# Kernel optimization log

Hardware: AMD Instinct MI355X
Metric: run time of the kernel (lower is better)

The kernel has to match this reference:

```python
import jax, jax.numpy as jnp
import numpy as np

BETA = 0.9      # membrane decay
THRESH = 1.0    # firing threshold


def _lif(x):
    """Leaky integrate-and-fire over leading time axis. x: (T, ..., C) -> spikes (T, ..., C)."""
    def step(mem, xt):
        mem = BETA * mem + xt
        s = (mem > THRESH).astype(xt.dtype)
        mem = mem - s * THRESH  # soft reset
        return mem, s
    _, spikes = jax.lax.scan(step, jnp.zeros_like(x[0]), x)
    return spikes


def setup_inputs() -> dict:
    key = jax.random.key(0)
    k1, k2, k3, k4, k5 = jax.random.split(key, 5)
    T, N, D = 4, 8192, 1024
    E, EF, TOPK = 8, 512, 2  # expert_ff = d_ff // n_experts = 4096 // 8
    x = jax.random.normal(k1, (T, N, D), dtype=jnp.float32)
    expert_indices = jax.random.randint(k2, (N, TOPK), 0, E)
    expert_weights = jax.random.uniform(k3, (N, TOPK), dtype=jnp.float32)
    up_w = jax.random.normal(k4, (E, EF, D), dtype=jnp.float32) * 0.02   # Linear(d_model, ef).weight
    down_w = jax.random.normal(k5, (E, D, EF), dtype=jnp.float32) * 0.02  # Linear(ef, d_model).weight
    return {"x": x, "expert_indices": expert_indices, "expert_weights": expert_weights,
            "up_w": up_w, "down_w": down_w}


def reference(x, expert_indices, expert_weights, up_w, down_w):
    T, N, D = x.shape
    E = up_w.shape[0]
    # Dense combine weights W[n, e] = sum_k weights[n, k] * (indices[n, k] == e)
    W = jnp.zeros((N, E), dtype=x.dtype).at[
        jnp.arange(N)[:, None], expert_indices].add(expert_weights)
    out = jnp.zeros_like(x)
    for e in range(E):  # fixed small loop over experts
        h = _lif(jnp.einsum('tnd,fd->tnf', x, up_w[e]))   # up-proj + LIF hidden
        o = _lif(jnp.einsum('tnf,df->tnd', h, down_w[e]))  # down-proj + LIF output
        out = out + o * W[:, e][None, :, None]             # weighted combine (0 for inactive)
    return out
```

## Files before the change

kernel.cpp:

```cpp
#include <hip/hip_runtime.h>
#include <stdint.h>

#define T_STEPS 4
#define NTOK    8192
#define DMODEL  1024
#define NEXP    8
#define EFF     512
#define BMT     128
#define CAPTOT  (2*NTOK + NEXP*BMT)

typedef __attribute__((ext_vector_type(8))) short bf8_t;
typedef __attribute__((ext_vector_type(4))) float f32x4;

#define MFMA(a,b,c) __builtin_amdgcn_mfma_f32_16x16x32_bf16((a),(b),(c),0,0,0)


__device__ __forceinline__ unsigned short bf16rn(float f) {
    unsigned u = __float_as_uint(f);
    unsigned r = u + 0x7fffu + ((u >> 16) & 1u);
    return (unsigned short)(r >> 16);
}
__device__ __forceinline__ float bf2f(unsigned short h) {
    return __uint_as_float(((unsigned)h) << 16);
}
__device__ __forceinline__ unsigned pk(unsigned short a, unsigned short b) {
    return (unsigned)a | ((unsigned)b << 16);
}

__device__ __forceinline__ void stage8_3limb(const float* __restrict__ src,
                                             unsigned short* d0, unsigned short* d1,
                                             unsigned short* d2) {
    float v[8];
    *(float4*)&v[0] = *(const float4*)(src + 0);
    *(float4*)&v[4] = *(const float4*)(src + 4);
    unsigned short h[8], m[8], l[8];
#pragma unroll
    for (int i = 0; i < 8; ++i) {
        unsigned short a = bf16rn(v[i]);
        float r1 = v[i] - bf2f(a);
        unsigned short b = bf16rn(r1);
        float r2 = r1 - bf2f(b);
        h[i] = a; m[i] = b; l[i] = bf16rn(r2);
    }
    *(uint4*)d0 = make_uint4(pk(h[0],h[1]), pk(h[2],h[3]), pk(h[4],h[5]), pk(h[6],h[7]));
    *(uint4*)d1 = make_uint4(pk(m[0],m[1]), pk(m[2],m[3]), pk(m[4],m[5]), pk(m[6],m[7]));
    *(uint4*)d2 = make_uint4(pk(l[0],l[1]), pk(l[2],l[3]), pk(l[4],l[5]), pk(l[6],l[7]));
}


__global__ void k_count(const int* __restrict__ idx, int* __restrict__ counts) {
    int n = blockIdx.x * blockDim.x + threadIdx.x;
    if (n >= NTOK) return;
    int e0 = idx[2*n], e1 = idx[2*n+1];
    atomicAdd(&counts[e0], 1);
    if (e1 != e0) atomicAdd(&counts[e1], 1);
}

__global__ void k_prefix(const int* __restrict__ counts, int* __restrict__ offsets) {
    if (threadIdx.x == 0) {
        int o = 0;
        for (int e = 0; e < NEXP; ++e) {
            offsets[e] = o;
            o += (counts[e] + BMT - 1) / BMT * BMT;
        }
        offsets[NEXP] = o;
    }
}

__global__ void k_fill(const int* __restrict__ idx, const float* __restrict__ wts,
                       const int* __restrict__ offsets, int* __restrict__ cursors,
                       int* __restrict__ tok, float* __restrict__ wgt) {
    int n = blockIdx.x * blockDim.x + threadIdx.x;
    if (n >= NTOK) return;
    int e0 = idx[2*n], e1 = idx[2*n+1];
    float w0 = wts[2*n], w1 = wts[2*n+1];
    if (e0 == e1) w0 = __fadd_rn(w0, w1);
    int p0 = offsets[e0] + atomicAdd(&cursors[e0], 1);
    tok[p0] = n; wgt[p0] = w0;
    if (e1 != e0) {
        int p1 = offsets[e1] + atomicAdd(&cursors[e1], 1);
        tok[p1] = n; wgt[p1] = w1;
    }
}


__global__ __launch_bounds__(256, 2)
void k_up(const float* __restrict__ x, const float* __restrict__ up_w,
          const int* __restrict__ offsets, const int* __restrict__ tok,
          unsigned short* __restrict__ spk) {
    const int m0 = blockIdx.x * BMT;
    const int ft = blockIdx.y;
    if (m0 >= offsets[NEXP]) return;
    int e = 0;
    for (int i = 1; i < NEXP; ++i) if (m0 >= offsets[i]) e = i;

    __shared__ unsigned short As[3][128][40];
    __shared__ unsigned short Bs[3][128][40];

    const int tid  = threadIdx.x;
    const int lane = tid & 63, wid = tid >> 6;
    const int quad = lane >> 4, l16 = lane & 15;
    const int mw = (wid & 1) * 64, nw = (wid >> 1) * 64;

    const int r = tid >> 1, half = tid & 1;
    const int tokA = tok[m0 + r];
    const float* xbase = x + (size_t)tokA * DMODEL + half * 16;
    const float* wrow  = up_w + ((size_t)e * EFF + ft * 128 + r) * DMODEL + half * 16;

    f32x4 mem[4][4];
#pragma unroll
    for (int i = 0; i < 4; ++i)
#pragma unroll
        for (int j = 0; j < 4; ++j) mem[i][j] = (f32x4){0.f,0.f,0.f,0.f};

    for (int t = 0; t < T_STEPS; ++t) {
        f32x4 acc[4][4];
#pragma unroll
        for (int i = 0; i < 4; ++i)
#pragma unroll
            for (int j = 0; j < 4; ++j) acc[i][j] = (f32x4){0.f,0.f,0.f,0.f};

        const float* xrow = xbase + (size_t)t * NTOK * DMODEL;

        for (int kc = 0; kc < DMODEL; kc += 32) {
            __syncthreads();
            stage8_3limb(xrow + kc,     &As[0][r][half*16],   &As[1][r][half*16],   &As[2][r][half*16]);
            stage8_3limb(xrow + kc + 8, &As[0][r][half*16+8], &As[1][r][half*16+8], &As[2][r][half*16+8]);
            stage8_3limb(wrow + kc,     &Bs[0][r][half*16],   &Bs[1][r][half*16],   &Bs[2][r][half*16]);
            stage8_3limb(wrow + kc + 8, &Bs[0][r][half*16+8], &Bs[1][r][half*16+8], &Bs[2][r][half*16+8]);
            __syncthreads();

            bf8_t bh[4], bm[4], bl[4];
#pragma unroll
            for (int nt = 0; nt < 4; ++nt) {
                const int nr = nw + nt*16 + l16;
                bh[nt] = *(const bf8_t*)&Bs[0][nr][quad*8];
                bm[nt] = *(const bf8_t*)&Bs[1][nr][quad*8];
                bl[nt] = *(const bf8_t*)&Bs[2][nr][quad*8];
            }
#pragma unroll
            for (int mt = 0; mt < 4; ++mt) {
                const int mr = mw + mt*16 + l16;
                bf8_t ah = *(const bf8_t*)&As[0][mr][quad*8];
                bf8_t am = *(const bf8_t*)&As[1][mr][quad*8];
                bf8_t al = *(const bf8_t*)&As[2][mr][quad*8];
#pragma unroll
                for (int nt = 0; nt < 4; ++nt) {
                    f32x4 c = acc[mt][nt];
                    c = MFMA(ah, bh[nt], c);
                    c = MFMA(am, bh[nt], c);
                    c = MFMA(ah, bm[nt], c);
                    c = MFMA(am, bm[nt], c);
                    c = MFMA(al, bh[nt], c);
                    c = MFMA(ah, bl[nt], c);
                    acc[mt][nt] = c;
                }
            }
        }

#pragma unroll
        for (int mt = 0; mt < 4; ++mt)
#pragma unroll
            for (int nt = 0; nt < 4; ++nt)
#pragma unroll
                for (int reg = 0; reg < 4; ++reg) {
                    float mv = __fadd_rn(__fmul_rn(0.9f, mem[mt][nt][reg]), acc[mt][nt][reg]);
                    bool s = mv > 1.0f;
                    mem[mt][nt][reg] = __fsub_rn(mv, s ? 1.0f : 0.0f);
                    int row = m0 + mw + mt*16 + quad*4 + reg;
                    int col = ft*128 + nw + nt*16 + l16;
                    spk[((size_t)t * CAPTOT + row) * EFF + col] = s ? 0x3F80u : 0u;
                }
    }
}


__global__ __launch_bounds__(256, 3)
void k_dn(const unsigned short* __restrict__ spk, const float* __restrict__ down_w,
          const int* __restrict__ offsets, const int* __restrict__ tok,
          const float* __restrict__ wgt, float* __restrict__ out) {
    const int m0 = blockIdx.x * BMT;
    const int dt = blockIdx.y;
    if (m0 >= offsets[NEXP]) return;
    int e = 0;
    for (int i = 1; i < NEXP; ++i) if (m0 >= offsets[i]) e = i;

    __shared__ unsigned short As[128][40];
    __shared__ unsigned short Bs[3][64][40];

    const int tid  = threadIdx.x;
    const int lane = tid & 63, wid = tid >> 6;
    const int quad = lane >> 4, l16 = lane & 15;
    const int mw = (wid & 1) * 64, nw = (wid >> 1) * 32;

    const int r = tid >> 1, half = tid & 1;
    const int dr = tid >> 2, q = tid & 3;
    const unsigned short* arow = spk + (size_t)(m0 + r) * EFF + half * 16;
    const float* brow = down_w + ((size_t)e * DMODEL + dt * 64 + dr) * EFF + q * 8;

    int   rn[4][4];
    float rw[4][4];
#pragma unroll
    for (int mt = 0; mt < 4; ++mt)
#pragma unroll
        for (int reg = 0; reg < 4; ++reg) {
            int rr = m0 + mw + mt*16 + quad*4 + reg;
            rn[mt][reg] = tok[rr];
            rw[mt][reg] = wgt[rr];
        }

    f32x4 mem[4][2];
#pragma unroll
    for (int i = 0; i < 4; ++i) { mem[i][0] = (f32x4){0.f,0.f,0.f,0.f}; mem[i][1] = (f32x4){0.f,0.f,0.f,0.f}; }

    for (int t = 0; t < T_STEPS; ++t) {
        f32x4 acc[4][2];
#pragma unroll
        for (int i = 0; i < 4; ++i) { acc[i][0] = (f32x4){0.f,0.f,0.f,0.f}; acc[i][1] = (f32x4){0.f,0.f,0.f,0.f}; }

        const unsigned short* at = arow + (size_t)t * CAPTOT * EFF;

        for (int kc = 0; kc < EFF; kc += 32) {
            __syncthreads();
            *(uint4*)&As[r][half*16 + 0] = *(const uint4*)(at + kc + 0);
            *(uint4*)&As[r][half*16 + 8] = *(const uint4*)(at + kc + 8);
            stage8_3limb(brow + kc, &Bs[0][dr][q*8], &Bs[1][dr][q*8], &Bs[2][dr][q*8]);
            __syncthreads();

            bf8_t bh[2], bm[2], bl[2];
#pragma unroll
            for (int nt = 0; nt < 2; ++nt) {
                const int nr = nw + nt*16 + l16;
                bh[nt] = *(const bf8_t*)&Bs[0][nr][quad*8];
                bm[nt] = *(const bf8_t*)&Bs[1][nr][quad*8];
                bl[nt] = *(const bf8_t*)&Bs[2][nr][quad*8];
            }
#pragma unroll
            for (int mt = 0; mt < 4; ++mt) {
                const int mr = mw + mt*16 + l16;
                bf8_t a = *(const bf8_t*)&As[mr][quad*8];
#pragma unroll
                for (int nt = 0; nt < 2; ++nt) {
                    f32x4 c = acc[mt][nt];
                    c = MFMA(a, bh[nt], c);
                    c = MFMA(a, bm[nt], c);
                    c = MFMA(a, bl[nt], c);
                    acc[mt][nt] = c;
                }
            }
        }

#pragma unroll
        for (int mt = 0; mt < 4; ++mt)
#pragma unroll
            for (int nt = 0; nt < 2; ++nt)
#pragma unroll
                for (int reg = 0; reg < 4; ++reg) {
                    float mv = __fadd_rn(__fmul_rn(0.9f, mem[mt][nt][reg]), acc[mt][nt][reg]);
                    bool s = mv > 1.0f;
                    mem[mt][nt][reg] = __fsub_rn(mv, s ? 1.0f : 0.0f);
                    float w = rw[mt][reg];
                    if (s && w != 0.0f) {
                        int col = dt*64 + nw + nt*16 + l16;
                        atomicAdd(out + ((size_t)t * NTOK + rn[mt][reg]) * DMODEL + col, w);
                    }
                }
    }
}


extern "C" void kernel_launch(void* const* d_in, const int* in_sizes, int n_in,
                              void* d_out, int out_size, void* d_ws, size_t ws_size,
                              hipStream_t stream) {
    const float* x      = (const float*)d_in[0];
    const int*   idx    = (const int*)  d_in[1];
    const float* wts    = (const float*)d_in[2];
    const float* up_w   = (const float*)d_in[3];
    const float* down_w = (const float*)d_in[4];
    float* out = (float*)d_out;

    char* ws = (char*)d_ws;
    int*   counts  = (int*)(ws + 0);
    int*   cursors = (int*)(ws + 32);
    int*   offsets = (int*)(ws + 64);
    int*   tok     = (int*)(ws + 128);
    float* wgt     = (float*)(ws + 128 + (size_t)CAPTOT * 4);
    unsigned short* spk = (unsigned short*)(ws + 128 + (size_t)CAPTOT * 8);

    hipMemsetAsync(ws, 0, 128 + (size_t)CAPTOT * 8, stream);
    hipMemsetAsync(out, 0, (size_t)out_size * sizeof(float), stream);

    k_count <<<(NTOK + 255) / 256, 256, 0, stream>>>(idx, counts);
    k_prefix<<<1, 64, 0, stream>>>(counts, offsets);
    k_fill  <<<(NTOK + 255) / 256, 256, 0, stream>>>(idx, wts, offsets, cursors, tok, wgt);

    dim3 gup(CAPTOT / BMT, EFF / 128);
    k_up<<<gup, 256, 0, stream>>>(x, up_w, offsets, tok, spk);

    dim3 gdn(CAPTOT / BMT, DMODEL / 64);
    k_dn<<<gdn, 256, 0, stream>>>(spk, down_w, offsets, tok, wgt, out);
}
```

Measured before the change: 1.053 ms.

## Pre-split inputs into bf16 limb planes and load MFMA operands directly from global

```diff
diff --git a/kernel.cpp b/kernel.cpp
--- a/kernel.cpp
+++ b/kernel.cpp
@@ -14,6 +14,22 @@
 
 #define MFMA(a,b,c) __builtin_amdgcn_mfma_f32_16x16x32_bf16((a),(b),(c),0,0,0)
 
+#define WS_TOK   128
+#define WS_WGT   (WS_TOK + CAPTOT*4)
+#define WS_SPK   (WS_WGT + CAPTOT*4)
+#define SPK_SZ   ((size_t)4*CAPTOT*EFF*2)
+#define WS_XH    (WS_SPK + SPK_SZ)
+#define XPL_SZ   ((size_t)T_STEPS*NTOK*DMODEL*2)
+#define WS_XM    (WS_XH + XPL_SZ)
+#define WS_XL    (WS_XM + XPL_SZ)
+#define WPL_SZ   ((size_t)NEXP*EFF*DMODEL*2)
+#define WS_UH    (WS_XL + XPL_SZ)
+#define WS_UM    (WS_UH + WPL_SZ)
+#define WS_UL    (WS_UM + WPL_SZ)
+#define WS_DH    (WS_UL + WPL_SZ)
+#define WS_DM    (WS_DH + WPL_SZ)
+#define WS_DL    (WS_DM + WPL_SZ)
+
 
 __device__ __forceinline__ unsigned short bf16rn(float f) {
     unsigned u = __float_as_uint(f);
@@ -27,24 +43,27 @@
     return (unsigned)a | ((unsigned)b << 16);
 }
 
-__device__ __forceinline__ void stage8_3limb(const float* __restrict__ src,
-                                             unsigned short* d0, unsigned short* d1,
-                                             unsigned short* d2) {
+__global__ __launch_bounds__(256)
+void k_split3(const float* __restrict__ in, unsigned short* __restrict__ ph,
+              unsigned short* __restrict__ pm, unsigned short* __restrict__ pl, int n8) {
+    int i = blockIdx.x * blockDim.x + threadIdx.x;
+    if (i >= n8) return;
+    const float* src = in + (size_t)i * 8;
     float v[8];
     *(float4*)&v[0] = *(const float4*)(src + 0);
     *(float4*)&v[4] = *(const float4*)(src + 4);
     unsigned short h[8], m[8], l[8];
 #pragma unroll
-    for (int i = 0; i < 8; ++i) {
-        unsigned short a = bf16rn(v[i]);
-        float r1 = v[i] - bf2f(a);
+    for (int j = 0; j < 8; ++j) {
+        unsigned short a = bf16rn(v[j]);
+        float r1 = v[j] - bf2f(a);
         unsigned short b = bf16rn(r1);
         float r2 = r1 - bf2f(b);
-        h[i] = a; m[i] = b; l[i] = bf16rn(r2);
-    }
-    *(uint4*)d0 = make_uint4(pk(h[0],h[1]), pk(h[2],h[3]), pk(h[4],h[5]), pk(h[6],h[7]));
-    *(uint4*)d1 = make_uint4(pk(m[0],m[1]), pk(m[2],m[3]), pk(m[4],m[5]), pk(m[6],m[7]));
-    *(uint4*)d2 = make_uint4(pk(l[0],l[1]), pk(l[2],l[3]), pk(l[4],l[5]), pk(l[6],l[7]));
+        h[j] = a; m[j] = b; l[j] = bf16rn(r2);
+    }
+    *(uint4*)(ph + (size_t)i*8) = make_uint4(pk(h[0],h[1]), pk(h[2],h[3]), pk(h[4],h[5]), pk(h[6],h[7]));
+    *(uint4*)(pm + (size_t)i*8) = make_uint4(pk(m[0],m[1]), pk(m[2],m[3]), pk(m[4],m[5]), pk(m[6],m[7]));
+    *(uint4*)(pl + (size_t)i*8) = make_uint4(pk(l[0],l[1]), pk(l[2],l[3]), pk(l[4],l[5]), pk(l[6],l[7]));
 }
 
 
@@ -85,7 +104,9 @@
 
 
 __global__ __launch_bounds__(256, 2)
-void k_up(const float* __restrict__ x, const float* __restrict__ up_w,
+void k_up(const unsigned short* __restrict__ xh, const unsigned short* __restrict__ xm,
+          const unsigned short* __restrict__ xl, const unsigned short* __restrict__ wh,
+          const unsigned short* __restrict__ wm, const unsigned short* __restrict__ wl,
           const int* __restrict__ offsets, const int* __restrict__ tok,
           unsigned short* __restrict__ spk) {
     const int m0 = blockIdx.x * BMT;
@@ -94,18 +115,17 @@
     int e = 0;
     for (int i = 1; i < NEXP; ++i) if (m0 >= offsets[i]) e = i;
 
-    __shared__ unsigned short As[3][128][40];
-    __shared__ unsigned short Bs[3][128][40];
-
-    const int tid  = threadIdx.x;
-    const int lane = tid & 63, wid = tid >> 6;
+    const int lane = threadIdx.x & 63, wid = threadIdx.x >> 6;
     const int quad = lane >> 4, l16 = lane & 15;
     const int mw = (wid & 1) * 64, nw = (wid >> 1) * 64;
 
-    const int r = tid >> 1, half = tid & 1;
-    const int tokA = tok[m0 + r];
-    const float* xbase = x + (size_t)tokA * DMODEL + half * 16;
-    const float* wrow  = up_w + ((size_t)e * EFF + ft * 128 + r) * DMODEL + half * 16;
+    unsigned aoff[4], boff[4];
+#pragma unroll
+    for (int mt = 0; mt < 4; ++mt)
+        aoff[mt] = (unsigned)tok[m0 + mw + mt*16 + l16] * DMODEL + quad*8;
+#pragma unroll
+    for (int nt = 0; nt < 4; ++nt)
+        boff[nt] = ((unsigned)e*EFF + ft*BMT + nw + nt*16 + l16) * DMODEL + quad*8;
 
     f32x4 mem[4][4];
 #pragma unroll
@@ -120,30 +140,21 @@
 #pragma unroll
             for (int j = 0; j < 4; ++j) acc[i][j] = (f32x4){0.f,0.f,0.f,0.f};
 
-        const float* xrow = xbase + (size_t)t * NTOK * DMODEL;
+        const unsigned xt = (unsigned)t * (NTOK * DMODEL);
 
         for (int kc = 0; kc < DMODEL; kc += 32) {
-            __syncthreads();
-            stage8_3limb(xrow + kc,     &As[0][r][half*16],   &As[1][r][half*16],   &As[2][r][half*16]);
-            stage8_3limb(xrow + kc + 8, &As[0][r][half*16+8], &As[1][r][half*16+8], &As[2][r][half*16+8]);
-            stage8_3limb(wrow + kc,     &Bs[0][r][half*16],   &Bs[1][r][half*16],   &Bs[2][r][half*16]);
-            stage8_3limb(wrow + kc + 8, &Bs[0][r][half*16+8], &Bs[1][r][half*16+8], &Bs[2][r][half*16+8]);
-            __syncthreads();
-
             bf8_t bh[4], bm[4], bl[4];
 #pragma unroll
             for (int nt = 0; nt < 4; ++nt) {
-                const int nr = nw + nt*16 + l16;
-                bh[nt] = *(const bf8_t*)&Bs[0][nr][quad*8];
-                bm[nt] = *(const bf8_t*)&Bs[1][nr][quad*8];
-                bl[nt] = *(const bf8_t*)&Bs[2][nr][quad*8];
+                bh[nt] = *(const bf8_t*)(wh + boff[nt] + kc);
+                bm[nt] = *(const bf8_t*)(wm + boff[nt] + kc);
+                bl[nt] = *(const bf8_t*)(wl + boff[nt] + kc);
             }
 #pragma unroll
             for (int mt = 0; mt < 4; ++mt) {
-                const int mr = mw + mt*16 + l16;
-                bf8_t ah = *(const bf8_t*)&As[0][mr][quad*8];
-                bf8_t am = *(const bf8_t*)&As[1][mr][quad*8];
-                bf8_t al = *(const bf8_t*)&As[2][mr][quad*8];
+                bf8_t ah = *(const bf8_t*)(xh + xt + aoff[mt] + kc);
+                bf8_t am = *(const bf8_t*)(xm + xt + aoff[mt] + kc);
+                bf8_t al = *(const bf8_t*)(xl + xt + aoff[mt] + kc);
 #pragma unroll
                 for (int nt = 0; nt < 4; ++nt) {
                     f32x4 c = acc[mt][nt];
@@ -168,15 +179,16 @@
                     bool s = mv > 1.0f;
                     mem[mt][nt][reg] = __fsub_rn(mv, s ? 1.0f : 0.0f);
                     int row = m0 + mw + mt*16 + quad*4 + reg;
-                    int col = ft*128 + nw + nt*16 + l16;
+                    int col = ft*BMT + nw + nt*16 + l16;
                     spk[((size_t)t * CAPTOT + row) * EFF + col] = s ? 0x3F80u : 0u;
                 }
     }
 }
 
 
-__global__ __launch_bounds__(256, 3)
-void k_dn(const unsigned short* __restrict__ spk, const float* __restrict__ down_w,
+__global__ __launch_bounds__(256, 2)
+void k_dn(const unsigned short* __restrict__ spk, const unsigned short* __restrict__ dh,
+          const unsigned short* __restrict__ dm, const unsigned short* __restrict__ dl,
           const int* __restrict__ offsets, const int* __restrict__ tok,
           const float* __restrict__ wgt, float* __restrict__ out) {
     const int m0 = blockIdx.x * BMT;
@@ -185,18 +197,17 @@
     int e = 0;
     for (int i = 1; i < NEXP; ++i) if (m0 >= offsets[i]) e = i;
 
-    __shared__ unsigned short As[128][40];
-    __shared__ unsigned short Bs[3][64][40];
-
-    const int tid  = threadIdx.x;
-    const int lane = tid & 63, wid = tid >> 6;
+    const int lane = threadIdx.x & 63, wid = threadIdx.x >> 6;
     const int quad = lane >> 4, l16 = lane & 15;
-    const int mw = (wid & 1) * 64, nw = (wid >> 1) * 32;
-
-    const int r = tid >> 1, half = tid & 1;
-    const int dr = tid >> 2, q = tid & 3;
-    const unsigned short* arow = spk + (size_t)(m0 + r) * EFF + half * 16;
-    const float* brow = down_w + ((size_t)e * DMODEL + dt * 64 + dr) * EFF + q * 8;
+    const int mw = (wid & 1) * 64, nw = (wid >> 1) * 64;
+
+    unsigned aoff[4], boff[4];
+#pragma unroll
+    for (int mt = 0; mt < 4; ++mt)
+        aoff[mt] = (unsigned)(m0 + mw + mt*16 + l16) * EFF + quad*8;
+#pragma unroll
+    for (int nt = 0; nt < 4; ++nt)
+        boff[nt] = ((unsigned)e*DMODEL + dt*BMT + nw + nt*16 + l16) * EFF + quad*8;
 
     int   rn[4][4];
     float rw[4][4];
@@ -209,38 +220,34 @@
             rw[mt][reg] = wgt[rr];
         }
 
-    f32x4 mem[4][2];
-#pragma unroll
-    for (int i = 0; i < 4; ++i) { mem[i][0] = (f32x4){0.f,0.f,0.f,0.f}; mem[i][1] = (f32x4){0.f,0.f,0.f,0.f}; }
+    f32x4 mem[4][4];
+#pragma unroll
+    for (int i = 0; i < 4; ++i)
+#pragma unroll
+        for (int j = 0; j < 4; ++j) mem[i][j] = (f32x4){0.f,0.f,0.f,0.f};
 
     for (int t = 0; t < T_STEPS; ++t) {
-        f32x4 acc[4][2];
-#pragma unroll
-        for (int i = 0; i < 4; ++i) { acc[i][0] = (f32x4){0.f,0.f,0.f,0.f}; acc[i][1] = (f32x4){0.f,0.f,0.f,0.f}; }
-
-        const unsigned short* at = arow + (size_t)t * CAPTOT * EFF;
+        f32x4 acc[4][4];
+#pragma unroll
+        for (int i = 0; i < 4; ++i)
+#pragma unroll
+            for (int j = 0; j < 4; ++j) acc[i][j] = (f32x4){0.f,0.f,0.f,0.f};
+
+        const unsigned st = (unsigned)t * (CAPTOT * EFF);
 
         for (int kc = 0; kc < EFF; kc += 32) {
-            __syncthreads();
-            *(uint4*)&As[r][half*16 + 0] = *(const uint4*)(at + kc + 0);
-            *(uint4*)&As[r][half*16 + 8] = *(const uint4*)(at + kc + 8);
-            stage8_3limb(brow + kc, &Bs[0][dr][q*8], &Bs[1][dr][q*8], &Bs[2][dr][q*8]);
-            __syncthreads();
-
-            bf8_t bh[2], bm[2], bl[2];
-#pragma unroll
-            for (int nt = 0; nt < 2; ++nt) {
-                const int nr = nw + nt*16 + l16;
-                bh[nt] = *(const bf8_t*)&Bs[0][nr][quad*8];
-                bm[nt] = *(const bf8_t*)&Bs[1][nr][quad*8];
-                bl[nt] = *(const bf8_t*)&Bs[2][nr][quad*8];
+            bf8_t bh[4], bm[4], bl[4];
+#pragma unroll
+            for (int nt = 0; nt < 4; ++nt) {
+                bh[nt] = *(const bf8_t*)(dh + boff[nt] + kc);
+                bm[nt] = *(const bf8_t*)(dm + boff[nt] + kc);
+                bl[nt] = *(const bf8_t*)(dl + boff[nt] + kc);
             }
 #pragma unroll
             for (int mt = 0; mt < 4; ++mt) {
-                const int mr = mw + mt*16 + l16;
-                bf8_t a = *(const bf8_t*)&As[mr][quad*8];
-#pragma unroll
-                for (int nt = 0; nt < 2; ++nt) {
+                bf8_t a = *(const bf8_t*)(spk + st + aoff[mt] + kc);
+#pragma unroll
+                for (int nt = 0; nt < 4; ++nt) {
                     f32x4 c = acc[mt][nt];
                     c = MFMA(a, bh[nt], c);
                     c = MFMA(a, bm[nt], c);
@@ -253,7 +260,7 @@
 #pragma unroll
         for (int mt = 0; mt < 4; ++mt)
 #pragma unroll
-            for (int nt = 0; nt < 2; ++nt)
+            for (int nt = 0; nt < 4; ++nt)
 #pragma unroll
                 for (int reg = 0; reg < 4; ++reg) {
                     float mv = __fadd_rn(__fmul_rn(0.9f, mem[mt][nt][reg]), acc[mt][nt][reg]);
@@ -261,7 +268,7 @@
                     mem[mt][nt][reg] = __fsub_rn(mv, s ? 1.0f : 0.0f);
                     float w = rw[mt][reg];
                     if (s && w != 0.0f) {
-                        int col = dt*64 + nw + nt*16 + l16;
+                        int col = dt*BMT + nw + nt*16 + l16;
                         atomicAdd(out + ((size_t)t * NTOK + rn[mt][reg]) * DMODEL + col, w);
                     }
                 }
@@ -283,20 +290,35 @@
     int*   counts  = (int*)(ws + 0);
     int*   cursors = (int*)(ws + 32);
     int*   offsets = (int*)(ws + 64);
-    int*   tok     = (int*)(ws + 128);
-    float* wgt     = (float*)(ws + 128 + (size_t)CAPTOT * 4);
-    unsigned short* spk = (unsigned short*)(ws + 128 + (size_t)CAPTOT * 8);
-
-    hipMemsetAsync(ws, 0, 128 + (size_t)CAPTOT * 8, stream);
+    int*   tok     = (int*)(ws + WS_TOK);
+    float* wgt     = (float*)(ws + WS_WGT);
+    unsigned short* spk = (unsigned short*)(ws + WS_SPK);
+    unsigned short* xh = (unsigned short*)(ws + WS_XH);
+    unsigned short* xm = (unsigned short*)(ws + WS_XM);
+    unsigned short* xl = (unsigned short*)(ws + WS_XL);
+    unsigned short* uh = (unsigned short*)(ws + WS_UH);
+    unsigned short* um = (unsigned short*)(ws + WS_UM);
+    unsigned short* ul = (unsigned short*)(ws + WS_UL);
+    unsigned short* dh = (unsigned short*)(ws + WS_DH);
+    unsigned short* dm = (unsigned short*)(ws + WS_DM);
+    unsigned short* dl = (unsigned short*)(ws + WS_DL);
+
+    hipMemsetAsync(ws, 0, WS_SPK, stream);
     hipMemsetAsync(out, 0, (size_t)out_size * sizeof(float), stream);
+
+    const int nx8 = T_STEPS*NTOK*DMODEL/8;
+    const int nw8 = NEXP*EFF*DMODEL/8;
+    k_split3<<<nx8/256, 256, 0, stream>>>(x, xh, xm, xl, nx8);
+    k_split3<<<nw8/256, 256, 0, stream>>>(up_w, uh, um, ul, nw8);
+    k_split3<<<nw8/256, 256, 0, stream>>>(down_w, dh, dm, dl, nw8);
 
     k_count <<<(NTOK + 255) / 256, 256, 0, stream>>>(idx, counts);
     k_prefix<<<1, 64, 0, stream>>>(counts, offsets);
     k_fill  <<<(NTOK + 255) / 256, 256, 0, stream>>>(idx, wts, offsets, cursors, tok, wgt);
 
-    dim3 gup(CAPTOT / BMT, EFF / 128);
-    k_up<<<gup, 256, 0, stream>>>(x, up_w, offsets, tok, spk);
-
-    dim3 gdn(CAPTOT / BMT, DMODEL / 64);
-    k_dn<<<gdn, 256, 0, stream>>>(spk, down_w, offsets, tok, wgt, out);
-}
+    dim3 gup(CAPTOT / BMT, EFF / BMT);
+    k_up<<<gup, 256, 0, stream>>>(xh, xm, xl, uh, um, ul, offsets, tok, spk);
+
+    dim3 gdn(CAPTOT / BMT, DMODEL / BMT);
+    k_dn<<<gdn, 256, 0, stream>>>(spk, dh, dm, dl, offsets, tok, wgt, out);
+}
```

Measured after the change: 1.652 ms. +56.9%, slower.
